# Optimization experiments

Hardware: AMD Instinct MI355X
Metric: run time of the kernel (lower is better)

Reference implementation:

```python
import jax, jax.numpy as jnp
import numpy as np

N = 50000
E = 800000
NEG_SLOPE = 0.2


def gatv2_layer(x, src, dst, Wl, Wr, att, bias, heads, ch):
    # x: [N, Fin]; Wl/Wr: [Fin, heads*ch]; att: [heads, ch]; bias: [heads*ch]
    xl = (x @ Wl).reshape(N, heads, ch)  # source transform
    xr = (x @ Wr).reshape(N, heads, ch)  # target transform
    e = xl[src] + xr[dst]                              # [E, H, C]
    s = jnp.einsum('ehc,hc->eh', jax.nn.leaky_relu(e, NEG_SLOPE), att)  # [E, H]
    # scatter-softmax over incoming edges of each target node
    smax = jax.ops.segment_max(s, dst, num_segments=N)  # [N, H]
    ex = jnp.exp(s - smax[dst])
    denom = jax.ops.segment_sum(ex, dst, num_segments=N)
    alpha = ex / denom[dst]                             # [E, H]
    out = jax.ops.segment_sum(xl[src] * alpha[..., None], dst, num_segments=N)  # [N, H, C]
    return out.reshape(N, heads * ch) + bias


def setup_inputs() -> dict:
    key = jax.random.key(0)
    ks = jax.random.split(key, 12)
    x = jax.random.normal(ks[0], (N, 128), dtype=jnp.float32)
    edge_index = jax.random.randint(ks[1], (2, E), 0, N, dtype=jnp.int64)
    edge_attr = jax.random.normal(ks[2], (E, 16), dtype=jnp.float32)
    s1 = 1.0 / np.sqrt(128.0)
    # layer 1: 128 -> 64, heads=2 (concat -> 128)
    Wl1 = jax.random.normal(ks[3], (128, 128), dtype=jnp.float32) * s1
    Wr1 = jax.random.normal(ks[4], (128, 128), dtype=jnp.float32) * s1
    att1 = jax.random.normal(ks[5], (2, 64), dtype=jnp.float32) * 0.1
    b1 = jnp.zeros((128,), dtype=jnp.float32)
    # layer 2: 128 -> 128, heads=1
    Wl2 = jax.random.normal(ks[6], (128, 128), dtype=jnp.float32) * s1
    Wr2 = jax.random.normal(ks[7], (128, 128), dtype=jnp.float32) * s1
    att2 = jax.random.normal(ks[8], (1, 128), dtype=jnp.float32) * 0.1
    b2 = jnp.zeros((128,), dtype=jnp.float32)
    return {"x": x, "edge_index": edge_index, "edge_attr": edge_attr,
            "Wl1": Wl1, "Wr1": Wr1, "att1": att1, "b1": b1,
            "Wl2": Wl2, "Wr2": Wr2, "att2": att2, "b2": b2}


def reference(x, edge_index, edge_attr, Wl1, Wr1, att1, b1, Wl2, Wr2, att2, b2):
    # using_edge_attr=False default path: edge_attr ignored.
    # GATv2Conv default add_self_loops=True
    loops = jnp.arange(N, dtype=edge_index.dtype)
    src = jnp.concatenate([edge_index[0], loops])
    dst = jnp.concatenate([edge_index[1], loops])
    h = gatv2_layer(x, src, dst, Wl1, Wr1, att1, b1, heads=2, ch=64)
    out = gatv2_layer(h, src, dst, Wl2, Wr2, att2, b2, heads=1, ch=128)
    return out
```

## Files before the change

kernel.cpp:

```cpp
#include <hip/hip_runtime.h>

#define NEG_SLOPE 0.2f
#define NPB 256
#define CHUNK 4096

typedef _Float16 f16x8 __attribute__((ext_vector_type(8)));
typedef _Float16 f16x4 __attribute__((ext_vector_type(4)));
typedef _Float16 f16x2 __attribute__((ext_vector_type(2)));
typedef float    f32x4 __attribute__((ext_vector_type(4)));

#if defined(__has_builtin)
#if __has_builtin(__builtin_amdgcn_fdot2)
#define HAVE_FDOT2 1
#endif
#endif

__device__ __forceinline__ f32x4 cvt4(f16x4 v) {
    return __builtin_convertvector(v, f32x4);
}

__global__ __launch_bounds__(256) void prep_kernel(
    const float* __restrict__ W0, const float* __restrict__ W1,
    const float* __restrict__ W2, const float* __restrict__ W3,
    _Float16* __restrict__ wt,
    const float* __restrict__ x, _Float16* __restrict__ xh,
    _Float16* __restrict__ xlo, int total, int* __restrict__ bcnt)
{
    int t = threadIdx.x;
    if (blockIdx.x < 256) {
        if (blockIdx.x == 0) bcnt[t] = 0;
        int idx = blockIdx.x * 256 + t;
        int m = idx >> 14;
        int k = (idx >> 7) & 127;
        int n = idx & 127;
        const float* W = (m == 0) ? W0 : (m == 1) ? W1 : (m == 2) ? W2 : W3;
        wt[m * 16384 + n * 128 + k] = (_Float16)W[k * 128 + n];
    } else {
        int i = (blockIdx.x - 256) * 256 + t;
        if (i * 2 < total) {
            float2 f = *(const float2*)(x + (size_t)i * 2);
            _Float16 h0 = (_Float16)f.x, h1 = (_Float16)f.y;
            _Float16 l0 = (_Float16)(f.x - (float)h0), l1 = (_Float16)(f.y - (float)h1);
            *(f16x2*)(xh  + (size_t)i * 2) = (f16x2){h0, h1};
            *(f16x2*)(xlo + (size_t)i * 2) = (f16x2){l0, l1};
        }
    }
}

__global__ __launch_bounds__(256) void gemm_f16_kernel(
    const _Float16* __restrict__ Ahi, const _Float16* __restrict__ Alo,
    const _Float16* __restrict__ Wt0, const _Float16* __restrict__ Wt1,
    _Float16* __restrict__ Cl, _Float16* __restrict__ Cr, int N)
{
    const _Float16* Wt = blockIdx.y ? Wt1 : Wt0;
    _Float16* C = blockIdx.y ? Cr : Cl;

    __shared__ _Float16 ldsW[128 * 136];

    const int tid = threadIdx.x;
    const int wave = tid >> 6;
    const int lane = tid & 63;
    const int mrow = lane & 15;
    const int quad = lane >> 4;
    const int rbase = blockIdx.x * 128 + wave * 32;

    const int sn = tid >> 1, shf = tid & 1;
    float4 stg[8];
    {
        const float4* g = (const float4*)(Wt + sn * 128 + shf * 64);
#pragma unroll
        for (int j = 0; j < 8; j++) stg[j] = g[j];
    }

    f16x8 ah[2][4], al[2][4];
#pragma unroll
    for (int rt = 0; rt < 2; rt++) {
        int r = rbase + rt * 16 + mrow;
        if (r > N - 1) r = N - 1;
        const _Float16* pa = Ahi + (size_t)r * 128 + quad * 8;
        const _Float16* pl = Alo + (size_t)r * 128 + quad * 8;
#pragma unroll
        for (int s = 0; s < 4; s++) {
            ah[rt][s] = *(const f16x8*)(pa + s * 32);
            al[rt][s] = *(const f16x8*)(pl + s * 32);
        }
    }

    {
        float4* d = (float4*)&ldsW[sn * 136 + shf * 64];
#pragma unroll
        for (int j = 0; j < 8; j++) d[j] = stg[j];
    }

    f32x4 acc[2][8];
#pragma unroll
    for (int rt = 0; rt < 2; rt++)
#pragma unroll
        for (int c = 0; c < 8; c++) acc[rt][c] = (f32x4){0.f, 0.f, 0.f, 0.f};

    __syncthreads();

#pragma unroll
    for (int s = 0; s < 4; s++) {
#pragma unroll
        for (int c = 0; c < 8; c++) {
            f16x8 bw = *(const f16x8*)&ldsW[(c * 16 + mrow) * 136 + s * 32 + quad * 8];
            acc[0][c] = __builtin_amdgcn_mfma_f32_16x16x32_f16(ah[0][s], bw, acc[0][c], 0, 0, 0);
            acc[0][c] = __builtin_amdgcn_mfma_f32_16x16x32_f16(al[0][s], bw, acc[0][c], 0, 0, 0);
            acc[1][c] = __builtin_amdgcn_mfma_f32_16x16x32_f16(ah[1][s], bw, acc[1][c], 0, 0, 0);
            acc[1][c] = __builtin_amdgcn_mfma_f32_16x16x32_f16(al[1][s], bw, acc[1][c], 0, 0, 0);
        }
    }

#pragma unroll
    for (int rt = 0; rt < 2; rt++)
#pragma unroll
        for (int i = 0; i < 4; i++) {
            int r = rbase + rt * 16 + quad * 4 + i;
            if (r < N) {
                _Float16* cr = C + (size_t)r * 128 + mrow;
#pragma unroll
                for (int c = 0; c < 8; c++) cr[c * 16] = (_Float16)acc[rt][c][i];
            }
        }
}

__global__ __launch_bounds__(256) void histB_kernel(
    const int* __restrict__ ei, int* __restrict__ bcnt, int E)
{
    __shared__ int bh[256];
    int t = threadIdx.x;
    bh[t] = 0;
    __syncthreads();
    int base = blockIdx.x * CHUNK;
#pragma unroll
    for (int j = 0; j < CHUNK / 256; j++) {
        int e = base + t + j * 256;
        if (e < E) atomicAdd(&bh[ei[E + e] >> 8], 1);
    }
    __syncthreads();
    if (bh[t]) atomicAdd(&bcnt[t], bh[t]);
}

__global__ __launch_bounds__(256) void scanB_kernel(
    const int* __restrict__ bcnt, int* __restrict__ bstart,
    int* __restrict__ gcursor, int NB, int E)
{
    __shared__ int s[256];
    int t = threadIdx.x;
    int v = (t < NB) ? bcnt[t] : 0;
    s[t] = v;
    __syncthreads();
    for (int off = 1; off < 256; off <<= 1) {
        int u = (t >= off) ? s[t - off] : 0;
        __syncthreads();
        s[t] += u;
        __syncthreads();
    }
    if (t < NB) { bstart[t] = s[t] - v; gcursor[t] = s[t] - v; }
    if (t == 0) bstart[NB] = E;
}

__global__ __launch_bounds__(256) void passA_kernel(
    const int* __restrict__ ei, int* __restrict__ gcursor,
    int2* __restrict__ staging, int E)
{
    __shared__ int bh[256];
    __shared__ int bbase[256];
    int t = threadIdx.x;
    bh[t] = 0;
    __syncthreads();
    int base = blockIdx.x * CHUNK;
    int srcv[16], dstv[16], rb[16];
#pragma unroll
    for (int j = 0; j < 16; j++) {
        int e = base + t + j * 256;
        if (e < E) {
            int d = ei[E + e];
            srcv[j] = ei[e];
            dstv[j] = d;
            int bk = d >> 8;
            int r = atomicAdd(&bh[bk], 1);
            rb[j] = (r << 8) | bk;
        } else rb[j] = -1;
    }
    __syncthreads();
    if (bh[t]) bbase[t] = atomicAdd(&gcursor[t], bh[t]);
    __syncthreads();
#pragma unroll
    for (int j = 0; j < 16; j++) {
        if (rb[j] >= 0) {
            int bk = rb[j] & 255, r = rb[j] >> 8;
            staging[bbase[bk] + r] = make_int2(srcv[j], dstv[j]);
        }
    }
}

__global__ __launch_bounds__(256) void passB_kernel(
    const int2* __restrict__ staging, const int* __restrict__ bstart,
    int* __restrict__ start, int* __restrict__ sorted_src, int N, int E)
{
    __shared__ int lhist[256], lscan[256], lcur[256];
    int b = blockIdx.x, t = threadIdx.x;
    int r0 = bstart[b], r1 = bstart[b + 1];
    lhist[t] = 0;
    __syncthreads();
    for (int i = r0 + t; i < r1; i += 256) atomicAdd(&lhist[staging[i].y & 255], 1);
    __syncthreads();
    int v = lhist[t];
    lscan[t] = v;
    __syncthreads();
    for (int off = 1; off < 256; off <<= 1) {
        int u = (t >= off) ? lscan[t - off] : 0;
        __syncthreads();
        lscan[t] += u;
        __syncthreads();
    }
    int excl = lscan[t] - v;
    int node = b * NPB + t;
    if (node < N) start[node] = r0 + excl;
    lcur[t] = excl;
    if (b == 0 && t == 0) start[N] = E;
    __syncthreads();
    for (int i = r0 + t; i < r1; i += 256) {
        int2 p = staging[i];
        int rank = atomicAdd(&lcur[p.y & 255], 1);
        sorted_src[r0 + rank] = p.x;
    }
}

template <int H, bool BFOUT>
__global__ __launch_bounds__(256) void gat_fused_kernel(
    const _Float16* __restrict__ xl, const _Float16* __restrict__ xr,
    const float* __restrict__ att, const float* __restrict__ bias,
    const int* __restrict__ start, const int* __restrict__ sorted_src,
    float* __restrict__ outf, _Float16* __restrict__ oh,
    _Float16* __restrict__ ol, int N)
{
    int node = blockIdx.x * 4 + (threadIdx.x >> 6);
    if (node >= N) return;
    const int lane = threadIdx.x & 63;
    const int half = lane >> 5;
    const int hl   = lane & 31;
    const int RED  = (H == 2) ? 8 : 16;
    const _Float16 NS = (_Float16)NEG_SLOPE;

    const f16x4 b4 = *(const f16x4*)(xr + (size_t)node * 128 + hl * 4);
    float4 attf = *(const float4*)(att + hl * 4);
    const float L2E = 1.44269504f;
    f16x4 av = {(_Float16)(attf.x * L2E), (_Float16)(attf.y * L2E),
                (_Float16)(attf.z * L2E), (_Float16)(attf.w * L2E)};
#if defined(HAVE_FDOT2)
    f16x2 avlo = __builtin_shufflevector(av, av, 0, 1);
    f16x2 avhi = __builtin_shufflevector(av, av, 2, 3);
#else
    f32x4 avf = cvt4(av);
#endif

#define SCORE(a_, p_) {                                                     \
        f16x4 t_ = (a_) + b4;                                               \
        f16x4 u_ = __builtin_elementwise_max(t_, t_ * NS);                  \
        _Float16 dummy_;                                                    \
        (void)dummy_;                                                       \
                                                \
        p_ = 0.f;                                                           \
        score_dot(u_, p_);                                                  \
    }

    auto score_dot = [&](f16x4 u_, float& p_) {
#if defined(HAVE_FDOT2)
        f16x2 ulo = __builtin_shufflevector(u_, u_, 0, 1);
        f16x2 uhi = __builtin_shufflevector(u_, u_, 2, 3);
        p_ = __builtin_amdgcn_fdot2(ulo, avlo,
             __builtin_amdgcn_fdot2(uhi, avhi, 0.0f, false), false);
#else
        f32x4 uf = cvt4(u_);
        p_ = uf[0] * avf[0] + uf[1] * avf[1] + uf[2] * avf[2] + uf[3] * avf[3];
#endif
    };

    f32x4 acc = (f32x4){0.f, 0.f, 0.f, 0.f};
    float den = 0.f;

    const int s0 = start[node];
    const int s1 = start[node + 1];
    const int M  = s1 - s0 + 1;
    const int Ksafe = (M - 1) >> 1;
    const int K     = (M + 1) >> 1;

    int k = 0;
    for (; k + 8 <= Ksafe; k += 8) {
        int src[8]; f16x4 a[8]; float p[8];
#pragma unroll
        for (int j = 0; j < 8; j++) {
            int iv = 2 * (k + j) + half;
            src[j] = (iv == 0) ? node : sorted_src[s0 + iv - 1];
        }
#pragma unroll
        for (int j = 0; j < 8; j++)
            a[j] = *(const f16x4*)(xl + (size_t)src[j] * 128 + hl * 4);
#pragma unroll
        for (int j = 0; j < 8; j++) SCORE(a[j], p[j]);
#pragma unroll
        for (int m = 1; m <= RED; m <<= 1) {
#pragma unroll
            for (int j = 0; j < 8; j++) p[j] += __shfl_xor(p[j], m, 64);
        }
#pragma unroll
        for (int j = 0; j < 8; j++) {
            float e = exp2f(p[j]);
            den += e;
            acc = acc + cvt4(a[j]) * e;
        }
    }
    for (; k + 4 <= Ksafe; k += 4) {
        int src[4]; f16x4 a[4]; float p[4];
#pragma unroll
        for (int j = 0; j < 4; j++) {
            int iv = 2 * (k + j) + half;
            src[j] = (iv == 0) ? node : sorted_src[s0 + iv - 1];
        }
#pragma unroll
        for (int j = 0; j < 4; j++)
            a[j] = *(const f16x4*)(xl + (size_t)src[j] * 128 + hl * 4);
#pragma unroll
        for (int j = 0; j < 4; j++) SCORE(a[j], p[j]);
#pragma unroll
        for (int m = 1; m <= RED; m <<= 1) {
#pragma unroll
            for (int j = 0; j < 4; j++) p[j] += __shfl_xor(p[j], m, 64);
        }
#pragma unroll
        for (int j = 0; j < 4; j++) {
            float e = exp2f(p[j]);
            den += e;
            acc = acc + cvt4(a[j]) * e;
        }
    }
    for (; k < Ksafe; k++) {
        int iv = 2 * k + half;
        int src = (iv == 0) ? node : sorted_src[s0 + iv - 1];
        f16x4 a = *(const f16x4*)(xl + (size_t)src * 128 + hl * 4);
        float p; SCORE(a, p);
#pragma unroll
        for (int m = 1; m <= RED; m <<= 1) p += __shfl_xor(p, m, 64);
        float e = exp2f(p);
        den += e;
        acc = acc + cvt4(a) * e;
    }
    for (; k < K; k++) {
        int iv = 2 * k + half;
        bool valid = iv < M;
        int pos = s0 + (iv > 0 ? iv - 1 : 0);
        int ld = sorted_src[pos];
        int src = (iv == 0) ? node : (valid ? ld : node);
        f16x4 a = *(const f16x4*)(xl + (size_t)src * 128 + hl * 4);
        float p; SCORE(a, p);
#pragma unroll
        for (int m = 1; m <= RED; m <<= 1) p += __shfl_xor(p, m, 64);
        float e = valid ? exp2f(p) : 0.f;
        den += e;
        acc = acc + cvt4(a) * e;
    }
#undef SCORE

    den    += __shfl_xor(den,    32, 64);
    acc[0] += __shfl_xor(acc[0], 32, 64);
    acc[1] += __shfl_xor(acc[1], 32, 64);
    acc[2] += __shfl_xor(acc[2], 32, 64);
    acc[3] += __shfl_xor(acc[3], 32, 64);

    float inv = 1.0f / den;
    float4 bi = *(const float4*)(bias + hl * 4);
    float o0 = acc[0] * inv + bi.x;
    float o1 = acc[1] * inv + bi.y;
    float o2 = acc[2] * inv + bi.z;
    float o3 = acc[3] * inv + bi.w;

    if (lane < 32) {
        if (BFOUT) {
            _Float16 h0 = (_Float16)o0, h1 = (_Float16)o1, h2 = (_Float16)o2, h3 = (_Float16)o3;
            f16x4 hv = {h0, h1, h2, h3};
            f16x4 lv = {(_Float16)(o0 - (float)h0), (_Float16)(o1 - (float)h1),
                        (_Float16)(o2 - (float)h2), (_Float16)(o3 - (float)h3)};
            *(f16x4*)(oh + (size_t)node * 128 + hl * 4) = hv;
            *(f16x4*)(ol + (size_t)node * 128 + hl * 4) = lv;
        } else {
            *(float4*)(outf + (size_t)node * 128 + hl * 4) = make_float4(o0, o1, o2, o3);
        }
    }
}

extern "C" void kernel_launch(void* const* d_in, const int* in_sizes, int n_in,
                              void* d_out, int out_size, void* d_ws, size_t ws_size,
                              hipStream_t stream)
{
    const float* x    = (const float*)d_in[0];
    const int*   ei   = (const int*)d_in[1];
    const float* Wl1  = (const float*)d_in[3];
    const float* Wr1  = (const float*)d_in[4];
    const float* att1 = (const float*)d_in[5];
    const float* b1   = (const float*)d_in[6];
    const float* Wl2  = (const float*)d_in[7];
    const float* Wr2  = (const float*)d_in[8];
    const float* att2 = (const float*)d_in[9];
    const float* b2   = (const float*)d_in[10];
    float* out = (float*)d_out;

    const int N  = in_sizes[0] / 128;
    const int E  = in_sizes[1] / 2;
    const int NB = (N + NPB - 1) / NPB;

    const size_t nf = (size_t)N * 128;
    _Float16* xlf  = (_Float16*)d_ws;
    _Float16* xrf  = xlf + nf;
    _Float16* ah   = xrf + nf;
    _Float16* al   = ah + nf;
    _Float16* wt   = al + nf;
    int* bcnt      = (int*)(wt + 4 * 16384);
    int* bstart    = bcnt + 256;
    int* gcursor   = bstart + 257;
    int* start     = gcursor + 256;
    size_t stgoff  = ((size_t)(start + N + 1) + 7) & ~(size_t)7;
    int2* staging  = (int2*)stgoff;
    int* sorted_src = (int*)(staging + E);

    const int grid_chunk = (E + CHUNK - 1) / CHUNK;
    const int node_grid  = (N + 3) / 4;
    const int gemm_gx    = (N + 127) / 128;
    const int split_grid = (int)((nf / 2 + 255) / 256);

    prep_kernel<<<256 + split_grid, 256, 0, stream>>>(
        Wl1, Wr1, Wl2, Wr2, wt, x, ah, al, (int)nf, bcnt);

    histB_kernel<<<grid_chunk, 256, 0, stream>>>(ei, bcnt, E);
    scanB_kernel<<<1, 256, 0, stream>>>(bcnt, bstart, gcursor, NB, E);
    passA_kernel<<<grid_chunk, 256, 0, stream>>>(ei, gcursor, staging, E);
    passB_kernel<<<NB, 256, 0, stream>>>(staging, bstart, start, sorted_src, N, E);

    gemm_f16_kernel<<<dim3(gemm_gx, 2), 256, 0, stream>>>(
        ah, al, wt + 0 * 16384, wt + 1 * 16384, xlf, xrf, N);
    gat_fused_kernel<2, true><<<node_grid, 256, 0, stream>>>(
        xlf, xrf, att1, b1, start, sorted_src, nullptr, ah, al, N);

    gemm_f16_kernel<<<dim3(gemm_gx, 2), 256, 0, stream>>>(
        ah, al, wt + 2 * 16384, wt + 3 * 16384, xlf, xrf, N);
    gat_fused_kernel<1, false><<<node_grid, 256, 0, stream>>>(
        xlf, xrf, att2, b2, start, sorted_src, out, nullptr, nullptr, N);
}
```

Baseline: 305.7 us.

## Split GAT edges across four 16-lane groups, merge histogram into prep kernel

```diff
diff --git a/kernel.cpp b/kernel.cpp
--- a/kernel.cpp
+++ b/kernel.cpp
@@ -13,30 +13,36 @@
 #if __has_builtin(__builtin_amdgcn_fdot2)
 #define HAVE_FDOT2 1
 #endif
-#endif
-
-__device__ __forceinline__ f32x4 cvt4(f16x4 v) {
-    return __builtin_convertvector(v, f32x4);
-}
+#if __has_builtin(__builtin_amdgcn_exp2f)
+#define EXP2F(v) __builtin_amdgcn_exp2f(v)
+#else
+#define EXP2F(v) exp2f(v)
+#endif
+#endif
+#ifndef EXP2F
+#define EXP2F(v) exp2f(v)
+#endif
 
 __global__ __launch_bounds__(256) void prep_kernel(
     const float* __restrict__ W0, const float* __restrict__ W1,
     const float* __restrict__ W2, const float* __restrict__ W3,
     _Float16* __restrict__ wt,
     const float* __restrict__ x, _Float16* __restrict__ xh,
-    _Float16* __restrict__ xlo, int total, int* __restrict__ bcnt)
-{
+    _Float16* __restrict__ xlo, int total, int nxblocks,
+    const int* __restrict__ ei, int* __restrict__ bcnt, int E)
+{
+    __shared__ int bh[256];
     int t = threadIdx.x;
-    if (blockIdx.x < 256) {
-        if (blockIdx.x == 0) bcnt[t] = 0;
-        int idx = blockIdx.x * 256 + t;
+    int bx = blockIdx.x;
+    if (bx < 256) {
+        int idx = bx * 256 + t;
         int m = idx >> 14;
         int k = (idx >> 7) & 127;
         int n = idx & 127;
         const float* W = (m == 0) ? W0 : (m == 1) ? W1 : (m == 2) ? W2 : W3;
         wt[m * 16384 + n * 128 + k] = (_Float16)W[k * 128 + n];
-    } else {
-        int i = (blockIdx.x - 256) * 256 + t;
+    } else if (bx < 256 + nxblocks) {
+        int i = (bx - 256) * 256 + t;
         if (i * 2 < total) {
             float2 f = *(const float2*)(x + (size_t)i * 2);
             _Float16 h0 = (_Float16)f.x, h1 = (_Float16)f.y;
@@ -44,6 +50,17 @@
             *(f16x2*)(xh  + (size_t)i * 2) = (f16x2){h0, h1};
             *(f16x2*)(xlo + (size_t)i * 2) = (f16x2){l0, l1};
         }
+    } else {
+        bh[t] = 0;
+        __syncthreads();
+        int base = (bx - 256 - nxblocks) * CHUNK;
+#pragma unroll
+        for (int j = 0; j < CHUNK / 256; j++) {
+            int e = base + t + j * 256;
+            if (e < E) atomicAdd(&bh[ei[E + e] >> 8], 1);
+        }
+        __syncthreads();
+        if (bh[t]) atomicAdd(&bcnt[t], bh[t]);
     }
 }
 
@@ -123,23 +140,6 @@
                 for (int c = 0; c < 8; c++) cr[c * 16] = (_Float16)acc[rt][c][i];
             }
         }
-}
-
-__global__ __launch_bounds__(256) void histB_kernel(
-    const int* __restrict__ ei, int* __restrict__ bcnt, int E)
-{
-    __shared__ int bh[256];
-    int t = threadIdx.x;
-    bh[t] = 0;
-    __syncthreads();
-    int base = blockIdx.x * CHUNK;
-#pragma unroll
-    for (int j = 0; j < CHUNK / 256; j++) {
-        int e = base + t + j * 256;
-        if (e < E) atomicAdd(&bh[ei[E + e] >> 8], 1);
-    }
-    __syncthreads();
-    if (bh[t]) atomicAdd(&bcnt[t], bh[t]);
 }
 
 __global__ __launch_bounds__(256) void scanB_kernel(
@@ -240,153 +240,146 @@
     int node = blockIdx.x * 4 + (threadIdx.x >> 6);
     if (node >= N) return;
     const int lane = threadIdx.x & 63;
-    const int half = lane >> 5;
-    const int hl   = lane & 31;
-    const int RED  = (H == 2) ? 8 : 16;
+    const int g    = lane >> 4;
+    const int cl   = lane & 15;
+    const int RED  = (H == 2) ? 4 : 8;
     const _Float16 NS = (_Float16)NEG_SLOPE;
-
-    const f16x4 b4 = *(const f16x4*)(xr + (size_t)node * 128 + hl * 4);
-    float4 attf = *(const float4*)(att + hl * 4);
     const float L2E = 1.44269504f;
-    f16x4 av = {(_Float16)(attf.x * L2E), (_Float16)(attf.y * L2E),
-                (_Float16)(attf.z * L2E), (_Float16)(attf.w * L2E)};
+
+    const f16x8 b8 = *(const f16x8*)(xr + (size_t)node * 128 + cl * 8);
+    f16x8 av;
+#pragma unroll
+    for (int i = 0; i < 8; i++) av[i] = (_Float16)(att[cl * 8 + i] * L2E);
 #if defined(HAVE_FDOT2)
-    f16x2 avlo = __builtin_shufflevector(av, av, 0, 1);
-    f16x2 avhi = __builtin_shufflevector(av, av, 2, 3);
+    f16x2 av0 = __builtin_shufflevector(av, av, 0, 1);
+    f16x2 av1 = __builtin_shufflevector(av, av, 2, 3);
+    f16x2 av2 = __builtin_shufflevector(av, av, 4, 5);
+    f16x2 av3 = __builtin_shufflevector(av, av, 6, 7);
+#endif
+
+    auto score = [&](f16x8 a) -> float {
+        f16x8 t = a + b8;
+        f16x8 u = __builtin_elementwise_max(t, t * NS);
+#if defined(HAVE_FDOT2)
+        float p = __builtin_amdgcn_fdot2(__builtin_shufflevector(u, u, 0, 1), av0, 0.0f, false);
+        p = __builtin_amdgcn_fdot2(__builtin_shufflevector(u, u, 2, 3), av1, p, false);
+        p = __builtin_amdgcn_fdot2(__builtin_shufflevector(u, u, 4, 5), av2, p, false);
+        p = __builtin_amdgcn_fdot2(__builtin_shufflevector(u, u, 6, 7), av3, p, false);
+        return p;
 #else
-    f32x4 avf = cvt4(av);
-#endif
-
-#define SCORE(a_, p_) {                                                     \
-        f16x4 t_ = (a_) + b4;                                               \
-        f16x4 u_ = __builtin_elementwise_max(t_, t_ * NS);                  \
-        _Float16 dummy_;                                                    \
-        (void)dummy_;                                                       \
-                                                \
-        p_ = 0.f;                                                           \
-        score_dot(u_, p_);                                                  \
-    }
-
-    auto score_dot = [&](f16x4 u_, float& p_) {
-#if defined(HAVE_FDOT2)
-        f16x2 ulo = __builtin_shufflevector(u_, u_, 0, 1);
-        f16x2 uhi = __builtin_shufflevector(u_, u_, 2, 3);
-        p_ = __builtin_amdgcn_fdot2(ulo, avlo,
-             __builtin_amdgcn_fdot2(uhi, avhi, 0.0f, false), false);
-#else
-        f32x4 uf = cvt4(u_);
-        p_ = uf[0] * avf[0] + uf[1] * avf[1] + uf[2] * avf[2] + uf[3] * avf[3];
+        float p = 0.f;
+#pragma unroll
+        for (int i = 0; i < 8; i++) p += (float)u[i] * (float)av[i];
+        return p;
 #endif
     };
 
-    f32x4 acc = (f32x4){0.f, 0.f, 0.f, 0.f};
+    float acc[8];
+#pragma unroll
+    for (int i = 0; i < 8; i++) acc[i] = 0.f;
     float den = 0.f;
 
     const int s0 = start[node];
     const int s1 = start[node + 1];
     const int M  = s1 - s0 + 1;
-    const int Ksafe = (M - 1) >> 1;
-    const int K     = (M + 1) >> 1;
-
-    int k = 0;
-    for (; k + 8 <= Ksafe; k += 8) {
-        int src[8]; f16x4 a[8]; float p[8];
-#pragma unroll
-        for (int j = 0; j < 8; j++) {
-            int iv = 2 * (k + j) + half;
-            src[j] = (iv == 0) ? node : sorted_src[s0 + iv - 1];
-        }
-#pragma unroll
-        for (int j = 0; j < 8; j++)
-            a[j] = *(const f16x4*)(xl + (size_t)src[j] * 128 + hl * 4);
-#pragma unroll
-        for (int j = 0; j < 8; j++) SCORE(a[j], p[j]);
+    const int Ksafe = M >> 2;
+    const int K     = (M + 3) >> 2;
+
+    {
+        int iv = g;
+        bool valid = iv < M;
+        int ld = sorted_src[s0 + (g > 0 ? g - 1 : 0)];
+        int src = (g == 0) ? node : (valid ? ld : node);
+        f16x8 a = *(const f16x8*)(xl + (size_t)src * 128 + cl * 8);
+        float p = score(a);
+#pragma unroll
+        for (int m = 1; m <= RED; m <<= 1) p += __shfl_xor(p, m, 64);
+        float e = valid ? EXP2F(p) : 0.f;
+        den += e;
+#pragma unroll
+        for (int i = 0; i < 8; i++) acc[i] += (float)a[i] * e;
+    }
+
+    int k = 1;
+    for (; k + 4 <= Ksafe; k += 4) {
+        int src[4]; f16x8 a[4]; float p[4];
+#pragma unroll
+        for (int j = 0; j < 4; j++)
+            src[j] = sorted_src[s0 + 4 * (k + j) + g - 1];
+#pragma unroll
+        for (int j = 0; j < 4; j++)
+            a[j] = *(const f16x8*)(xl + (size_t)src[j] * 128 + cl * 8);
+#pragma unroll
+        for (int j = 0; j < 4; j++) p[j] = score(a[j]);
 #pragma unroll
         for (int m = 1; m <= RED; m <<= 1) {
 #pragma unroll
-            for (int j = 0; j < 8; j++) p[j] += __shfl_xor(p[j], m, 64);
-        }
-#pragma unroll
-        for (int j = 0; j < 8; j++) {
-            float e = exp2f(p[j]);
+            for (int j = 0; j < 4; j++) p[j] += __shfl_xor(p[j], m, 64);
+        }
+#pragma unroll
+        for (int j = 0; j < 4; j++) {
+            float e = EXP2F(p[j]);
             den += e;
-            acc = acc + cvt4(a[j]) * e;
-        }
-    }
-    for (; k + 4 <= Ksafe; k += 4) {
-        int src[4]; f16x4 a[4]; float p[4];
-#pragma unroll
-        for (int j = 0; j < 4; j++) {
-            int iv = 2 * (k + j) + half;
-            src[j] = (iv == 0) ? node : sorted_src[s0 + iv - 1];
-        }
-#pragma unroll
-        for (int j = 0; j < 4; j++)
-            a[j] = *(const f16x4*)(xl + (size_t)src[j] * 128 + hl * 4);
-#pragma unroll
-        for (int j = 0; j < 4; j++) SCORE(a[j], p[j]);
-#pragma unroll
-        for (int m = 1; m <= RED; m <<= 1) {
-#pragma unroll
-            for (int j = 0; j < 4; j++) p[j] += __shfl_xor(p[j], m, 64);
-        }
-#pragma unroll
-        for (int j = 0; j < 4; j++) {
-            float e = exp2f(p[j]);
-            den += e;
-            acc = acc + cvt4(a[j]) * e;
+#pragma unroll
+            for (int i = 0; i < 8; i++) acc[i] += (float)a[j][i] * e;
         }
     }
     for (; k < Ksafe; k++) {
-        int iv = 2 * k + half;
-        int src = (iv == 0) ? node : sorted_src[s0 + iv - 1];
-        f16x4 a = *(const f16x4*)(xl + (size_t)src * 128 + hl * 4);
-        float p; SCORE(a, p);
+        int src = sorted_src[s0 + 4 * k + g - 1];
+        f16x8 a = *(const f16x8*)(xl + (size_t)src * 128 + cl * 8);
+        float p = score(a);
 #pragma unroll
         for (int m = 1; m <= RED; m <<= 1) p += __shfl_xor(p, m, 64);
-        float e = exp2f(p);
+        float e = EXP2F(p);
         den += e;
-        acc = acc + cvt4(a) * e;
+#pragma unroll
+        for (int i = 0; i < 8; i++) acc[i] += (float)a[i] * e;
     }
     for (; k < K; k++) {
-        int iv = 2 * k + half;
+        int iv = 4 * k + g;
         bool valid = iv < M;
-        int pos = s0 + (iv > 0 ? iv - 1 : 0);
-        int ld = sorted_src[pos];
-        int src = (iv == 0) ? node : (valid ? ld : node);
-        f16x4 a = *(const f16x4*)(xl + (size_t)src * 128 + hl * 4);
-        float p; SCORE(a, p);
+        int ld = sorted_src[s0 + iv - 1];
+        int src = valid ? ld : node;
+        f16x8 a = *(const f16x8*)(xl + (size_t)src * 128 + cl * 8);
+        float p = score(a);
 #pragma unroll
         for (int m = 1; m <= RED; m <<= 1) p += __shfl_xor(p, m, 64);
-        float e = valid ? exp2f(p) : 0.f;
+        float e = valid ? EXP2F(p) : 0.f;
         den += e;
-        acc = acc + cvt4(a) * e;
-    }
-#undef SCORE
-
-    den    += __shfl_xor(den,    32, 64);
-    acc[0] += __shfl_xor(acc[0], 32, 64);
-    acc[1] += __shfl_xor(acc[1], 32, 64);
-    acc[2] += __shfl_xor(acc[2], 32, 64);
-    acc[3] += __shfl_xor(acc[3], 32, 64);
+#pragma unroll
+        for (int i = 0; i < 8; i++) acc[i] += (float)a[i] * e;
+    }
+
+    den += __shfl_xor(den, 16, 64);
+    den += __shfl_xor(den, 32, 64);
+#pragma unroll
+    for (int i = 0; i < 8; i++) {
+        acc[i] += __shfl_xor(acc[i], 16, 64);
+        acc[i] += __shfl_xor(acc[i], 32, 64);
+    }
 
     float inv = 1.0f / den;
-    float4 bi = *(const float4*)(bias + hl * 4);
-    float o0 = acc[0] * inv + bi.x;
-    float o1 = acc[1] * inv + bi.y;
-    float o2 = acc[2] * inv + bi.z;
-    float o3 = acc[3] * inv + bi.w;
-
-    if (lane < 32) {
+    if (lane < 16) {
+        float o[8];
+        float4 bi0 = *(const float4*)(bias + cl * 8);
+        float4 bi1 = *(const float4*)(bias + cl * 8 + 4);
+        o[0] = acc[0] * inv + bi0.x; o[1] = acc[1] * inv + bi0.y;
+        o[2] = acc[2] * inv + bi0.z; o[3] = acc[3] * inv + bi0.w;
+        o[4] = acc[4] * inv + bi1.x; o[5] = acc[5] * inv + bi1.y;
+        o[6] = acc[6] * inv + bi1.z; o[7] = acc[7] * inv + bi1.w;
         if (BFOUT) {
-            _Float16 h0 = (_Float16)o0, h1 = (_Float16)o1, h2 = (_Float16)o2, h3 = (_Float16)o3;
-            f16x4 hv = {h0, h1, h2, h3};
-            f16x4 lv = {(_Float16)(o0 - (float)h0), (_Float16)(o1 - (float)h1),
-                        (_Float16)(o2 - (float)h2), (_Float16)(o3 - (float)h3)};
-            *(f16x4*)(oh + (size_t)node * 128 + hl * 4) = hv;
-            *(f16x4*)(ol + (size_t)node * 128 + hl * 4) = lv;
+            f16x8 hv, lv;
+#pragma unroll
+            for (int i = 0; i < 8; i++) {
+                _Float16 h = (_Float16)o[i];
+                hv[i] = h;
+                lv[i] = (_Float16)(o[i] - (float)h);
+            }
+            *(f16x8*)(oh + (size_t)node * 128 + cl * 8) = hv;
+            *(f16x8*)(ol + (size_t)node * 128 + cl * 8) = lv;
         } else {
-            *(float4*)(outf + (size_t)node * 128 + hl * 4) = make_float4(o0, o1, o2, o3);
+            *(float4*)(outf + (size_t)node * 128 + cl * 8)     = make_float4(o[0], o[1], o[2], o[3]);
+            *(float4*)(outf + (size_t)node * 128 + cl * 8 + 4) = make_float4(o[4], o[5], o[6], o[7]);
         }
     }
 }
@@ -430,10 +423,10 @@
     const int gemm_gx    = (N + 127) / 128;
     const int split_grid = (int)((nf / 2 + 255) / 256);
 
-    prep_kernel<<<256 + split_grid, 256, 0, stream>>>(
-        Wl1, Wr1, Wl2, Wr2, wt, x, ah, al, (int)nf, bcnt);
-
-    histB_kernel<<<grid_chunk, 256, 0, stream>>>(ei, bcnt, E);
+    hipMemsetAsync(bcnt, 0, 256 * sizeof(int), stream);
+    prep_kernel<<<256 + split_grid + grid_chunk, 256, 0, stream>>>(
+        Wl1, Wr1, Wl2, Wr2, wt, x, ah, al, (int)nf, split_grid, ei, bcnt, E);
+
     scanB_kernel<<<1, 256, 0, stream>>>(bcnt, bstart, gcursor, NB, E);
     passA_kernel<<<grid_chunk, 256, 0, stream>>>(ei, gcursor, staging, E);
     passB_kernel<<<NB, 256, 0, stream>>>(staging, bstart, start, sorted_src, N, E);
```

After: 341.2 us. 11.6% more time.
